# Kernel tuning notes

Measured on AMD Instinct MI355X. Metric: run time of the kernel, lower is better.

## Reference

```python
import jax, jax.numpy as jnp
import numpy as np

S = 16384          # vision tokens (one image, 128x128 patches)
HID = 1280         # vision_hidden_size
H = 16             # num heads
D = HID // H       # head_dim = 80
L = 8              # vision_depth
FF = 3456          # vision_intermediate_size
WIN = 64           # tokens per attention window
UNIT = 4           # spatial_merge_size ** 2
OUT = 2048         # vision_out_hidden_size
PV = 3 * 2 * 16 * 16  # patch volume = 1536


def setup_inputs() -> dict:
    keys = iter(jax.random.split(jax.random.key(0), 32))
    def nrm(shape, fan_in):
        return jax.random.normal(next(keys), shape, jnp.float32) * (fan_in ** -0.5)
    ang = jax.random.uniform(next(keys), (S, D // 2), jnp.float32, 0.0, 2.0 * float(np.pi))
    ang = jnp.concatenate([ang, ang], axis=-1)  # rotate_half-compatible duplicated layout
    return {
        "x": jax.random.normal(next(keys), (S, PV), jnp.float32),
        "cos": jnp.cos(ang), "sin": jnp.sin(ang),
        "cu_seqlens": jnp.arange(S // WIN + 1, dtype=jnp.int32) * WIN,
        "pe_w": nrm((PV, HID), PV), "pe_b": jnp.zeros((HID,), jnp.float32),
        "ln1_w": jnp.ones((L, HID), jnp.float32), "ln1_b": jnp.zeros((L, HID), jnp.float32),
        "qkv_w": nrm((L, HID, 3 * HID), HID), "qkv_b": jnp.zeros((L, 3 * HID), jnp.float32),
        "proj_w": nrm((L, HID, HID), HID), "proj_b": jnp.zeros((L, HID), jnp.float32),
        "ln2_w": jnp.ones((L, HID), jnp.float32), "ln2_b": jnp.zeros((L, HID), jnp.float32),
        "fc1_w": nrm((L, HID, FF), HID), "fc1_b": jnp.zeros((L, FF), jnp.float32),
        "fc2_w": nrm((L, FF, HID), FF), "fc2_b": jnp.zeros((L, HID), jnp.float32),
        "m_ln_w": jnp.ones((HID,), jnp.float32), "m_ln_b": jnp.zeros((HID,), jnp.float32),
        "m_fc1_w": nrm((UNIT * HID, UNIT * HID), UNIT * HID), "m_fc1_b": jnp.zeros((UNIT * HID,), jnp.float32),
        "m_fc2_w": nrm((UNIT * HID, OUT), UNIT * HID), "m_fc2_b": jnp.zeros((OUT,), jnp.float32),
    }


def _ln(t, w, b, eps=1e-6):
    m = jnp.mean(t, axis=-1, keepdims=True)
    v = jnp.mean((t - m) ** 2, axis=-1, keepdims=True)
    return (t - m) * jax.lax.rsqrt(v + eps) * w + b


def _forward(cu_seqlens, x, cos, sin, pe_w, pe_b, ln1_w, ln1_b, qkv_w, qkv_b,
             proj_w, proj_b, ln2_w, ln2_b, fc1_w, fc1_b, fc2_w, fc2_b,
             m_ln_w, m_ln_b, m_fc1_w, m_fc1_b, m_fc2_w, m_fc2_b):
    NW = cu_seqlens.shape[0] - 1  # uniform windows (static)
    W = S // NW
    scale = D ** -0.5
    cosr = cos[:, None, :]  # [S,1,D]
    sinr = sin[:, None, :]

    def rope(t):  # t: [S,H,D]
        t1, t2 = jnp.split(t, 2, axis=-1)
        return t * cosr + jnp.concatenate((-t2, t1), axis=-1) * sinr

    h = x @ pe_w + pe_b  # patch embed: [S, HID]

    def block(h, p):
        l1w, l1b, qw, qb, pw, pb, l2w, l2b, f1w, f1b, f2w, f2b = p
        xn = _ln(h, l1w, l1b)
        q, k, v = jnp.split(xn @ qw + qb, 3, axis=-1)
        q = rope(q.reshape(S, H, D))
        k = rope(k.reshape(S, H, D))
        v = v.reshape(S, H, D)
        # block-diagonal (windowed) attention, fp32 scores as in source
        qw_ = q.reshape(NW, W, H, D)
        kw_ = k.reshape(NW, W, H, D)
        vw_ = v.reshape(NW, W, H, D)
        scores = jnp.einsum('wqhd,wkhd->whqk', qw_, kw_) * scale
        attn = jnp.einsum('whqk,wkhd->wqhd', jax.nn.softmax(scores, axis=-1), vw_)
        h = h + (attn.reshape(S, HID) @ pw + pb)
        xn2 = _ln(h, l2w, l2b)
        h = h + (jax.nn.gelu(xn2 @ f1w + f1b, approximate=True) @ f2w + f2b)
        return h, None

    h, _ = jax.lax.scan(block, h, (ln1_w, ln1_b, qkv_w, qkv_b, proj_w, proj_b,
                                   ln2_w, ln2_b, fc1_w, fc1_b, fc2_w, fc2_b))
    # patch merger (pre-shuffle norm)
    hm = _ln(h, m_ln_w, m_ln_b).reshape(-1, UNIT * HID)  # [S/4, 5120]
    return jax.nn.gelu(hm @ m_fc1_w + m_fc1_b, approximate=True) @ m_fc2_w + m_fc2_b


def reference(x, cos, sin, cu_seqlens, pe_w, pe_b, ln1_w, ln1_b, qkv_w, qkv_b,
              proj_w, proj_b, ln2_w, ln2_b, fc1_w, fc1_b, fc2_w, fc2_b,
              m_ln_w, m_ln_b, m_fc1_w, m_fc1_b, m_fc2_w, m_fc2_b):
    return _forward(cu_seqlens, x, cos, sin, pe_w, pe_b, ln1_w, ln1_b, qkv_w, qkv_b,
                    proj_w, proj_b, ln2_w, ln2_b, fc1_w, fc1_b, fc2_w, fc2_b,
                    m_ln_w, m_ln_b, m_fc1_w, m_fc1_b, m_fc2_w, m_fc2_b)
```

## Files before the change

### kernel.cpp

```cpp
#include <hip/hip_runtime.h>

typedef unsigned short ushortT;
typedef __attribute__((ext_vector_type(8))) short short8;
typedef __attribute__((ext_vector_type(8))) unsigned short ushort8;
typedef __attribute__((ext_vector_type(4))) unsigned short ushort4v;
typedef __attribute__((ext_vector_type(4))) float f32x4;

#define DEVINL __device__ __forceinline__

DEVINL ushortT f2bf(float f) {
    unsigned u = __builtin_bit_cast(unsigned, f);
    u += 0x7FFFu + ((u >> 16) & 1u);
    return (ushortT)(u >> 16);
}
DEVINL float bf2f(ushortT h) {
    unsigned u = ((unsigned)h) << 16;
    return __builtin_bit_cast(float, u);
}
DEVINL float gelu_tanh(float x) {
    float x3 = x * x * x;
    return 0.5f * x * (1.0f + tanhf(0.7978845608028654f * (x + 0.044715f * x3)));
}

#define GLOAD_LDS16(g, l)                                                     \
    __builtin_amdgcn_global_load_lds(                                         \
        (const __attribute__((address_space(1))) void*)(g),                   \
        (__attribute__((address_space(3))) void*)(l), 16, 0, 0)

__global__ __launch_bounds__(256) void cast_bf16_4(const float* __restrict__ in,
                                                   ushortT* __restrict__ out, long n4) {
    long i = (long)blockIdx.x * 256 + threadIdx.x;
    if (i < n4) {
        const float* p = in + i * 4;
        ushort4v o;
        o[0] = f2bf(p[0]); o[1] = f2bf(p[1]); o[2] = f2bf(p[2]); o[3] = f2bf(p[3]);
        ((ushort4v*)out)[i] = o;
    }
}

__global__ __launch_bounds__(256) void transpose_cast(const float* __restrict__ in,
                                                      ushortT* __restrict__ out,
                                                      int K, int N, int Npad) {
    __shared__ float tile[32][33];
    long zi = (long)blockIdx.z * K * N;
    long zo = (long)blockIdx.z * Npad * K;
    const float* ip = in + zi;
    ushortT* op = out + zo;
    int t = threadIdx.x, bx = blockIdx.x, by = blockIdx.y;
#pragma unroll
    for (int i = 0; i < 4; i++) {
        int idx = i * 256 + t, r = idx >> 5, c = idx & 31;
        int col = bx * 32 + c;
        tile[r][c] = (col < N) ? ip[(long)(by * 32 + r) * N + col] : 0.0f;
    }
    __syncthreads();
#pragma unroll
    for (int i = 0; i < 4; i++) {
        int idx = i * 256 + t, r = idx >> 5, c = idx & 31;
        op[(long)(bx * 32 + r) * K + by * 32 + c] = f2bf(tile[c][r]);
    }
}

__global__ __launch_bounds__(256) void pad_bias(const float* __restrict__ in,
                                                float* __restrict__ out,
                                                int n_in, int n_out, int total) {
    int i = blockIdx.x * 256 + threadIdx.x;
    if (i < total) {
        int l = i / n_out, c = i % n_out;
        out[i] = (c < n_in) ? in[l * n_in + c] : 0.0f;
    }
}

__global__ __launch_bounds__(256) void ln_to_bf16(const float* __restrict__ in,
                                                  const float* __restrict__ w,
                                                  const float* __restrict__ b,
                                                  ushortT* __restrict__ out) {
    const int row = blockIdx.x;
    const float* x = in + (long)row * 1280;
    __shared__ float red[4];
    float v[5];
    float s = 0.f;
#pragma unroll
    for (int i = 0; i < 5; i++) { v[i] = x[threadIdx.x + i * 256]; s += v[i]; }
#pragma unroll
    for (int o = 32; o > 0; o >>= 1) s += __shfl_xor(s, o);
    int wave = threadIdx.x >> 6;
    if ((threadIdx.x & 63) == 0) red[wave] = s;
    __syncthreads();
    float mean = (red[0] + red[1] + red[2] + red[3]) * (1.0f / 1280.0f);
    float q = 0.f;
#pragma unroll
    for (int i = 0; i < 5; i++) { float d = v[i] - mean; q += d * d; }
#pragma unroll
    for (int o = 32; o > 0; o >>= 1) q += __shfl_xor(q, o);
    __syncthreads();
    if ((threadIdx.x & 63) == 0) red[wave] = q;
    __syncthreads();
    float var = (red[0] + red[1] + red[2] + red[3]) * (1.0f / 1280.0f);
    float rs = rsqrtf(var + 1e-6f);
#pragma unroll
    for (int i = 0; i < 5; i++) {
        int c = threadIdx.x + i * 256;
        out[(long)row * 1280 + c] = f2bf((v[i] - mean) * rs * w[c] + b[c]);
    }
}

template <int BM, int BN, int WN, bool OBF, bool RES, bool GEL>
__global__ __launch_bounds__(128 * WN, WN == 4 ? 2 : 3)
void gemm2ph(const ushortT* __restrict__ A, const ushortT* __restrict__ Bt,
             const float* __restrict__ bias, const float* __restrict__ res,
             void* __restrict__ out, int M, int N, int K, int lda, int ldb) {
    constexpr int THREADS = 128 * WN;
    constexpr int MR = BM / 32;
    constexpr int NR = BN / (WN * 16);
    constexpr int AOPS = (BM * 8) / THREADS;
    constexpr int BOPS = (BN * 8) / THREADS;
    __shared__ ushortT lsA[2][BM * 64];
    __shared__ ushortT lsB[2][BN * 64];

    const int t = threadIdx.x;
    const int lane = t & 63, lr = lane & 15, lg = lane >> 4;
    const int wave = t >> 6;
    const int wr = wave / WN, wc = wave % WN;

    const int nwg = gridDim.x;
    const int orig = blockIdx.x;
    const int q = nwg >> 3, r8 = nwg & 7;
    const int xcd = orig & 7, loc = orig >> 3;
    const int wg = (xcd < r8 ? xcd * (q + 1) : r8 * (q + 1) + (xcd - r8) * q) + loc;
    const int gx = N / BN;
    const int bx = wg % gx, by = wg / gx;
    const long brow = (long)by * BM;
    const long bcol = (long)bx * BN;

    auto stage = [&](int buf, int k0) {
#pragma unroll
        for (int j = 0; j < AOPS; j++) {
            int idx = j * THREADS + t;
            int row = idx >> 3, slot = idx & 7;
            int ss = slot ^ (row & 7);
            GLOAD_LDS16(A + (size_t)(brow + row) * lda + k0 + ss * 8,
                        &lsA[buf][idx * 8]);
        }
#pragma unroll
        for (int j = 0; j < BOPS; j++) {
            int idx = j * THREADS + t;
            int row = idx >> 3, slot = idx & 7;
            int ss = slot ^ (row & 7);
            GLOAD_LDS16(Bt + (size_t)(bcol + row) * ldb + k0 + ss * 8,
                        &lsB[buf][idx * 8]);
        }
    };

    f32x4 acc[MR][NR];
#pragma unroll
    for (int m = 0; m < MR; m++)
#pragma unroll
        for (int n = 0; n < NR; n++) acc[m][n] = f32x4{0.f, 0.f, 0.f, 0.f};

    stage(0, 0);
    __syncthreads();

    const int NT = K >> 6;
    for (int tt = 0; tt < NT; tt++) {
        const int cur = tt & 1;
        if (tt + 1 < NT) stage(cur ^ 1, (tt + 1) << 6);
#pragma unroll
        for (int kk = 0; kk < 2; kk++) {
            short8 af[MR], bfg[NR];
#pragma unroll
            for (int m = 0; m < MR; m++) {
                int row = wr * (BM / 2) + m * 16 + lr;
                af[m] = *(const short8*)&lsA[cur][row * 64 + (((kk * 4 + lg) ^ (row & 7)) * 8)];
            }
#pragma unroll
            for (int n = 0; n < NR; n++) {
                int row = wc * (BN / WN) + n * 16 + lr;
                bfg[n] = *(const short8*)&lsB[cur][row * 64 + (((kk * 4 + lg) ^ (row & 7)) * 8)];
            }
#pragma unroll
            for (int m = 0; m < MR; m++)
#pragma unroll
                for (int n = 0; n < NR; n++)
                    acc[m][n] = __builtin_amdgcn_mfma_f32_16x16x32_bf16(af[m], bfg[n],
                                                                        acc[m][n], 0, 0, 0);
        }
        __syncthreads();
    }

#pragma unroll
    for (int m = 0; m < MR; m++) {
#pragma unroll
        for (int n = 0; n < NR; n++) {
#pragma unroll
            for (int rr = 0; rr < 4; rr++) {
                size_t row = brow + wr * (BM / 2) + m * 16 + lg * 4 + rr;
                size_t col = bcol + wc * (BN / WN) + n * 16 + lr;
                float v = acc[m][n][rr] + bias[col];
                if (RES) v += res[row * N + col];
                if (GEL) v = gelu_tanh(v);
                if (OBF) ((ushortT*)out)[row * N + col] = f2bf(v);
                else     ((float*)out)[row * N + col] = v;
            }
        }
    }
}

__global__ __launch_bounds__(256) void attn_win(const ushortT* __restrict__ qkv,
                                                const float* __restrict__ cosb,
                                                const float* __restrict__ sinb,
                                                ushortT* __restrict__ out) {
    const int w = blockIdx.x, h = blockIdx.y;
    __shared__ ushortT qs[64 * 96];
    __shared__ ushortT ks[64 * 96];
    __shared__ ushortT vt[80 * 80];
    __shared__ float   sc[64 * 65];
    __shared__ ushortT pb[64 * 80];
    const int t = threadIdx.x, wave = t >> 6, lane = t & 63, lr = lane & 15, lg = lane >> 4;
    const ushortT* bq = qkv + (long)w * 64 * 3840 + h * 80;

    for (int c = t; c < 640; c += 256) {
        int r = c / 10, cb = c % 10;
        const ushortT* qp = bq + (long)r * 3840;
        ushort8 qa = *(const ushort8*)(qp + cb * 8);
        ushort8 ka = *(const ushort8*)(qp + 1280 + cb * 8);
        int pcb = (cb < 5) ? cb + 5 : cb - 5;
        ushort8 qpr = *(const ushort8*)(qp + pcb * 8);
        ushort8 kpr = *(const ushort8*)(qp + 1280 + pcb * 8);
        long srow = (long)w * 64 + r;
        const float* cp = cosb + srow * 80 + cb * 8;
        const float* sp = sinb + srow * 80 + cb * 8;
        float sgn = (cb < 5) ? -1.f : 1.f;
        ushort8 qo, ko;
#pragma unroll
        for (int j = 0; j < 8; j++) {
            float c_ = cp[j], s_ = sp[j] * sgn;
            qo[j] = f2bf(bf2f(qa[j]) * c_ + bf2f(qpr[j]) * s_);
            ko[j] = f2bf(bf2f(ka[j]) * c_ + bf2f(kpr[j]) * s_);
        }
        *(ushort8*)&qs[r * 96 + cb * 8] = qo;
        *(ushort8*)&ks[r * 96 + cb * 8] = ko;
        ushort8 vv = *(const ushort8*)(qp + 2560 + cb * 8);
#pragma unroll
        for (int j = 0; j < 8; j++) vt[(cb * 8 + j) * 80 + r] = vv[j];
    }
    for (int idx = t; idx < 1024; idx += 256) {
        int r = idx >> 4, c2 = 80 + (idx & 15);
        qs[r * 96 + c2] = 0;
        ks[r * 96 + c2] = 0;
    }
    __syncthreads();

    f32x4 sa[4];
#pragma unroll
    for (int n = 0; n < 4; n++) sa[n] = f32x4{0.f, 0.f, 0.f, 0.f};
#pragma unroll
    for (int kk = 0; kk < 3; kk++) {
        short8 aq = *(const short8*)&qs[(wave * 16 + lr) * 96 + kk * 32 + lg * 8];
#pragma unroll
        for (int n = 0; n < 4; n++) {
            short8 bk = *(const short8*)&ks[(n * 16 + lr) * 96 + kk * 32 + lg * 8];
            sa[n] = __builtin_amdgcn_mfma_f32_16x16x32_bf16(aq, bk, sa[n], 0, 0, 0);
        }
    }
    const float scale = 0.11180339887498949f;
#pragma unroll
    for (int n = 0; n < 4; n++)
#pragma unroll
        for (int r = 0; r < 4; r++)
            sc[(wave * 16 + lg * 4 + r) * 65 + n * 16 + lr] = sa[n][r] * scale;
    __syncthreads();

    {
        int row = t >> 2, q4 = t & 3;
        float pv[16];
        float mx = -1e30f;
#pragma unroll
        for (int j = 0; j < 16; j++) { pv[j] = sc[row * 65 + q4 * 16 + j]; mx = fmaxf(mx, pv[j]); }
        mx = fmaxf(mx, __shfl_xor(mx, 1));
        mx = fmaxf(mx, __shfl_xor(mx, 2));
        float sum = 0.f;
#pragma unroll
        for (int j = 0; j < 16; j++) { pv[j] = __expf(pv[j] - mx); sum += pv[j]; }
        sum += __shfl_xor(sum, 1);
        sum += __shfl_xor(sum, 2);
        float inv = 1.0f / sum;
#pragma unroll
        for (int j = 0; j < 16; j++) pb[row * 80 + q4 * 16 + j] = f2bf(pv[j] * inv);
    }
    __syncthreads();

    f32x4 pa[5];
#pragma unroll
    for (int n = 0; n < 5; n++) pa[n] = f32x4{0.f, 0.f, 0.f, 0.f};
#pragma unroll
    for (int kk = 0; kk < 2; kk++) {
        short8 ap = *(const short8*)&pb[(wave * 16 + lr) * 80 + kk * 32 + lg * 8];
#pragma unroll
        for (int n = 0; n < 5; n++) {
            short8 bv = *(const short8*)&vt[(n * 16 + lr) * 80 + kk * 32 + lg * 8];
            pa[n] = __builtin_amdgcn_mfma_f32_16x16x32_bf16(ap, bv, pa[n], 0, 0, 0);
        }
    }
    ushortT* ob = out + (long)w * 64 * 1280 + h * 80;
#pragma unroll
    for (int n = 0; n < 5; n++)
#pragma unroll
        for (int r = 0; r < 4; r++)
            ob[(long)(wave * 16 + lg * 4 + r) * 1280 + n * 16 + lr] = f2bf(pa[n][r]);
}

extern "C" void kernel_launch(void* const* d_in, const int* in_sizes, int n_in,
                              void* d_out, int out_size, void* d_ws, size_t ws_size,
                              hipStream_t stream) {
    const float* x      = (const float*)d_in[0];
    const float* cosb   = (const float*)d_in[1];
    const float* sinb   = (const float*)d_in[2];
    const float* pe_w   = (const float*)d_in[4];
    const float* pe_b   = (const float*)d_in[5];
    const float* ln1_w  = (const float*)d_in[6];
    const float* ln1_b  = (const float*)d_in[7];
    const float* qkv_w  = (const float*)d_in[8];
    const float* qkv_b  = (const float*)d_in[9];
    const float* proj_w = (const float*)d_in[10];
    const float* proj_b = (const float*)d_in[11];
    const float* ln2_w  = (const float*)d_in[12];
    const float* ln2_b  = (const float*)d_in[13];
    const float* fc1_w  = (const float*)d_in[14];
    const float* fc1_b  = (const float*)d_in[15];
    const float* fc2_w  = (const float*)d_in[16];
    const float* fc2_b  = (const float*)d_in[17];
    const float* mln_w  = (const float*)d_in[18];
    const float* mln_b  = (const float*)d_in[19];
    const float* mfc1_w = (const float*)d_in[20];
    const float* mfc1_b = (const float*)d_in[21];
    const float* mfc2_w = (const float*)d_in[22];
    const float* mfc2_b = (const float*)d_in[23];

    char* ws = (char*)d_ws;
    size_t off = 0;
    auto alloc = [&](size_t bytes) -> char* {
        char* p = ws + off;
        off += (bytes + 255) & ~(size_t)255;
        return p;
    };
    ushortT* pe_wT   = (ushortT*)alloc((size_t)1280 * 1536 * 2);
    ushortT* qkv_wT  = (ushortT*)alloc((size_t)8 * 3840 * 1280 * 2);
    ushortT* proj_wT = (ushortT*)alloc((size_t)8 * 1280 * 1280 * 2);
    ushortT* fc1_wT  = (ushortT*)alloc((size_t)8 * 3584 * 1280 * 2);
    ushortT* fc2_wT  = (ushortT*)alloc((size_t)8 * 1280 * 3456 * 2);
    ushortT* mfc1_wT = (ushortT*)alloc((size_t)5120 * 5120 * 2);
    ushortT* mfc2_wT = (ushortT*)alloc((size_t)2048 * 5120 * 2);
    float*   fc1_bp  = (float*)alloc((size_t)8 * 3584 * 4);
    float*   hbuf    = (float*)alloc((size_t)16384 * 1280 * 4);
    ushortT* xn      = (ushortT*)alloc((size_t)16384 * 1280 * 2);
    ushortT* big     = (ushortT*)alloc((size_t)16384 * 3840 * 2);
    ushortT* attnb   = (ushortT*)alloc((size_t)16384 * 1280 * 2);

    ushortT* xbf  = big;
    ushortT* qkvb = big;
    ushortT* ffn1 = big;
    ushortT* t1   = attnb;

    transpose_cast<<<dim3(1280 / 32, 1536 / 32, 1), 256, 0, stream>>>(pe_w,   pe_wT,   1536, 1280, 1280);
    transpose_cast<<<dim3(3840 / 32, 1280 / 32, 8), 256, 0, stream>>>(qkv_w,  qkv_wT,  1280, 3840, 3840);
    transpose_cast<<<dim3(1280 / 32, 1280 / 32, 8), 256, 0, stream>>>(proj_w, proj_wT, 1280, 1280, 1280);
    transpose_cast<<<dim3(3584 / 32, 1280 / 32, 8), 256, 0, stream>>>(fc1_w,  fc1_wT,  1280, 3456, 3584);
    transpose_cast<<<dim3(1280 / 32, 3456 / 32, 8), 256, 0, stream>>>(fc2_w,  fc2_wT,  3456, 1280, 1280);
    transpose_cast<<<dim3(5120 / 32, 5120 / 32, 1), 256, 0, stream>>>(mfc1_w, mfc1_wT, 5120, 5120, 5120);
    transpose_cast<<<dim3(2048 / 32, 5120 / 32, 1), 256, 0, stream>>>(mfc2_w, mfc2_wT, 5120, 2048, 2048);
    pad_bias<<<(8 * 3584 + 255) / 256, 256, 0, stream>>>(fc1_b, fc1_bp, 3456, 3584, 8 * 3584);

    cast_bf16_4<<<(16384L * 1536 / 4 + 255) / 256, 256, 0, stream>>>(x, xbf, 16384L * 1536 / 4);
    gemm2ph<128, 128, 2, false, false, false><<<dim3(10 * 128), 256, 0, stream>>>(
        xbf, pe_wT, pe_b, nullptr, hbuf, 16384, 1280, 1536, 1536, 1536);

    for (int l = 0; l < 8; l++) {
        ln_to_bf16<<<16384, 256, 0, stream>>>(hbuf, ln1_w + l * 1280, ln1_b + l * 1280, xn);
        gemm2ph<256, 256, 4, true, false, false><<<dim3(15 * 64), 512, 0, stream>>>(
            xn, qkv_wT + (size_t)l * 3840 * 1280, qkv_b + l * 3840, nullptr, qkvb,
            16384, 3840, 1280, 1280, 1280);
        attn_win<<<dim3(256, 16), 256, 0, stream>>>(qkvb, cosb, sinb, attnb);
        gemm2ph<128, 128, 2, false, true, false><<<dim3(10 * 128), 256, 0, stream>>>(
            attnb, proj_wT + (size_t)l * 1280 * 1280, proj_b + l * 1280, hbuf, hbuf,
            16384, 1280, 1280, 1280, 1280);
        ln_to_bf16<<<16384, 256, 0, stream>>>(hbuf, ln2_w + l * 1280, ln2_b + l * 1280, xn);
        gemm2ph<256, 256, 4, true, false, true><<<dim3(14 * 64), 512, 0, stream>>>(
            xn, fc1_wT + (size_t)l * 3584 * 1280, fc1_bp + l * 3584, nullptr, ffn1,
            16384, 3584, 1280, 1280, 1280);
        gemm2ph<128, 128, 2, false, true, false><<<dim3(10 * 128), 256, 0, stream>>>(
            ffn1, fc2_wT + (size_t)l * 1280 * 3456, fc2_b + l * 1280, hbuf, hbuf,
            16384, 1280, 3456, 3584, 3456);
    }

    ln_to_bf16<<<16384, 256, 0, stream>>>(hbuf, mln_w, mln_b, xn);
    gemm2ph<128, 128, 2, true, false, true><<<dim3(40 * 32), 256, 0, stream>>>(
        xn, mfc1_wT, mfc1_b, nullptr, t1, 4096, 5120, 5120, 5120, 5120);
    gemm2ph<128, 128, 2, false, false, false><<<dim3(16 * 32), 256, 0, stream>>>(
        t1, mfc2_wT, mfc2_b, nullptr, (float*)d_out, 4096, 2048, 5120, 5120, 5120);
}
```

Before: 7.741 ms.

## Replace GEMM with 8-phase pipelined 256x256 kernel using fine-grained waits

Replaces the double-buffered gemm2ph template with a fixed 256x256 tile, 8-wave kernel. The K-loop is split into four quarter-phases that interleave half-tile global-to-LDS loads with MFMA work, using explicit vmcnt/lgkmcnt waits, raw barriers, sched barriers and setprio around the MFMA bursts. All GEMMs, including the N=1280 and N=2048 ones, now use 256x256 tiles. This hides load latency better but cuts the grid size for the narrow GEMMs (320 or 128 workgroups), which risks poorer CU occupancy on those launches.

```diff
diff --git a/kernel.cpp b/kernel.cpp
--- a/kernel.cpp
+++ b/kernel.cpp
@@ -26,6 +26,12 @@
     __builtin_amdgcn_global_load_lds(                                         \
         (const __attribute__((address_space(1))) void*)(g),                   \
         (__attribute__((address_space(3))) void*)(l), 16, 0, 0)
+
+#define WAITV(n) asm volatile("s_waitcnt vmcnt(" #n ")" ::: "memory")
+#define LGKM0() asm volatile("s_waitcnt lgkmcnt(0)" ::: "memory")
+#define MEMFENCE() asm volatile("" ::: "memory")
+#define BAR() __builtin_amdgcn_s_barrier()
+#define SCHEDBAR() __builtin_amdgcn_sched_barrier(0)
 
 __global__ __launch_bounds__(256) void cast_bf16_4(const float* __restrict__ in,
                                                    ushortT* __restrict__ out, long n4) {
@@ -105,97 +111,128 @@
     }
 }
 
-template <int BM, int BN, int WN, bool OBF, bool RES, bool GEL>
-__global__ __launch_bounds__(128 * WN, WN == 4 ? 2 : 3)
-void gemm2ph(const ushortT* __restrict__ A, const ushortT* __restrict__ Bt,
+
+#define STAGE_A(buf, half, k0)                                                \
+    _Pragma("unroll") for (int j = 0; j < 2; j++) {                           \
+        int c = j * 512 + t; int sr = c >> 3, slot = c & 7;                   \
+        size_t grow = (size_t)((sr & 63) + ((sr >> 6) << 7) + (half) * 64);   \
+        GLOAD_LDS16(A + (brow + grow) * lda + (k0) + ((slot ^ (sr & 7)) * 8), \
+                    &lsA[buf][(half) * 8192 + c * 8]);                        \
+    }
+#define STAGE_B(buf, half, k0)                                                \
+    _Pragma("unroll") for (int j = 0; j < 2; j++) {                           \
+        int c = j * 512 + t; int sr = c >> 3, slot = c & 7;                   \
+        size_t grow = (size_t)((sr & 31) + ((sr >> 5) << 6) + (half) * 32);   \
+        GLOAD_LDS16(Bt + (bcol + grow) * ldb + (k0) + ((slot ^ (sr & 7)) * 8),\
+                    &lsB[buf][(half) * 8192 + c * 8]);                        \
+    }
+#define READ_A(half)                                                          \
+    _Pragma("unroll") for (int m = 0; m < 4; m++)                             \
+    _Pragma("unroll") for (int kk = 0; kk < 2; kk++) {                        \
+        int sr = wr * 64 + m * 16 + lr;                                       \
+        aF[m][kk] = *(const short8*)&lsA[p][(half) * 8192 + sr * 64 +         \
+                                            (((kk * 4 + lg) ^ (sr & 7)) * 8)];\
+    }
+#define READ_B(nbase)                                                         \
+    _Pragma("unroll") for (int n = 0; n < 2; n++)                             \
+    _Pragma("unroll") for (int kk = 0; kk < 2; kk++) {                        \
+        int sr = wc * 32 + n * 16 + lr;                                       \
+        bF[(nbase) + n][kk] = *(const short8*)&lsB[p][((nbase) >> 1) * 8192 + \
+                                sr * 64 + (((kk * 4 + lg) ^ (sr & 7)) * 8)];  \
+    }
+#define MFMA_Q(half, nbase)                                                   \
+    __builtin_amdgcn_s_setprio(1);                                            \
+    _Pragma("unroll") for (int kk = 0; kk < 2; kk++)                          \
+    _Pragma("unroll") for (int m = 0; m < 4; m++)                             \
+    _Pragma("unroll") for (int n = 0; n < 2; n++)                             \
+        acc[(half) * 4 + m][(nbase) + n] = __builtin_amdgcn_mfma_f32_16x16x32_bf16( \
+            aF[m][kk], bF[(nbase) + n][kk], acc[(half) * 4 + m][(nbase) + n], 0, 0, 0); \
+    __builtin_amdgcn_s_setprio(0);
+
+#define PRE_MFMA() BAR(); LGKM0(); SCHEDBAR()
+
+template <bool OBF, bool RES, bool GEL>
+__global__ __launch_bounds__(512, 2)
+void gemm8ph(const ushortT* __restrict__ A, const ushortT* __restrict__ Bt,
              const float* __restrict__ bias, const float* __restrict__ res,
              void* __restrict__ out, int M, int N, int K, int lda, int ldb) {
-    constexpr int THREADS = 128 * WN;
-    constexpr int MR = BM / 32;
-    constexpr int NR = BN / (WN * 16);
-    constexpr int AOPS = (BM * 8) / THREADS;
-    constexpr int BOPS = (BN * 8) / THREADS;
-    __shared__ ushortT lsA[2][BM * 64];
-    __shared__ ushortT lsB[2][BN * 64];
-
+    __shared__ ushortT lsA[2][16384];
+    __shared__ ushortT lsB[2][16384];
     const int t = threadIdx.x;
     const int lane = t & 63, lr = lane & 15, lg = lane >> 4;
     const int wave = t >> 6;
-    const int wr = wave / WN, wc = wave % WN;
-
-    const int nwg = gridDim.x;
-    const int orig = blockIdx.x;
+    const int wr = wave >> 2, wc = wave & 3;
+
+    const int nwg = gridDim.x, orig = blockIdx.x;
     const int q = nwg >> 3, r8 = nwg & 7;
     const int xcd = orig & 7, loc = orig >> 3;
     const int wg = (xcd < r8 ? xcd * (q + 1) : r8 * (q + 1) + (xcd - r8) * q) + loc;
-    const int gx = N / BN;
-    const int bx = wg % gx, by = wg / gx;
-    const long brow = (long)by * BM;
-    const long bcol = (long)bx * BN;
-
-    auto stage = [&](int buf, int k0) {
-#pragma unroll
-        for (int j = 0; j < AOPS; j++) {
-            int idx = j * THREADS + t;
-            int row = idx >> 3, slot = idx & 7;
-            int ss = slot ^ (row & 7);
-            GLOAD_LDS16(A + (size_t)(brow + row) * lda + k0 + ss * 8,
-                        &lsA[buf][idx * 8]);
-        }
-#pragma unroll
-        for (int j = 0; j < BOPS; j++) {
-            int idx = j * THREADS + t;
-            int row = idx >> 3, slot = idx & 7;
-            int ss = slot ^ (row & 7);
-            GLOAD_LDS16(Bt + (size_t)(bcol + row) * ldb + k0 + ss * 8,
-                        &lsB[buf][idx * 8]);
-        }
-    };
-
-    f32x4 acc[MR][NR];
-#pragma unroll
-    for (int m = 0; m < MR; m++)
-#pragma unroll
-        for (int n = 0; n < NR; n++) acc[m][n] = f32x4{0.f, 0.f, 0.f, 0.f};
-
-    stage(0, 0);
-    __syncthreads();
-
+    const int gx = N >> 8;
+    const size_t brow = (size_t)(wg / gx) * 256;
+    const size_t bcol = (size_t)(wg % gx) * 256;
+
+    f32x4 acc[8][4];
+#pragma unroll
+    for (int m = 0; m < 8; m++)
+#pragma unroll
+        for (int n = 0; n < 4; n++) acc[m][n] = f32x4{0.f, 0.f, 0.f, 0.f};
+
+    STAGE_A(0, 0, 0);
+    STAGE_B(0, 0, 0);
+    STAGE_A(0, 1, 0);
+    STAGE_B(0, 1, 0);
+    WAITV(4); BAR(); MEMFENCE();
+
+    short8 aF[4][2], bF[4][2];
     const int NT = K >> 6;
-    for (int tt = 0; tt < NT; tt++) {
-        const int cur = tt & 1;
-        if (tt + 1 < NT) stage(cur ^ 1, (tt + 1) << 6);
-#pragma unroll
-        for (int kk = 0; kk < 2; kk++) {
-            short8 af[MR], bfg[NR];
-#pragma unroll
-            for (int m = 0; m < MR; m++) {
-                int row = wr * (BM / 2) + m * 16 + lr;
-                af[m] = *(const short8*)&lsA[cur][row * 64 + (((kk * 4 + lg) ^ (row & 7)) * 8)];
-            }
-#pragma unroll
-            for (int n = 0; n < NR; n++) {
-                int row = wc * (BN / WN) + n * 16 + lr;
-                bfg[n] = *(const short8*)&lsB[cur][row * 64 + (((kk * 4 + lg) ^ (row & 7)) * 8)];
-            }
-#pragma unroll
-            for (int m = 0; m < MR; m++)
-#pragma unroll
-                for (int n = 0; n < NR; n++)
-                    acc[m][n] = __builtin_amdgcn_mfma_f32_16x16x32_bf16(af[m], bfg[n],
-                                                                        acc[m][n], 0, 0, 0);
-        }
-        __syncthreads();
-    }
-
-#pragma unroll
-    for (int m = 0; m < MR; m++) {
-#pragma unroll
-        for (int n = 0; n < NR; n++) {
+    int p = 0;
+    for (int tt = 0; tt < NT - 1; ++tt) {
+        const int k1 = (tt + 1) << 6;
+        READ_A(0); READ_B(0);
+        STAGE_A(p ^ 1, 0, k1);
+        PRE_MFMA();
+        MFMA_Q(0, 0);
+        WAITV(4); BAR(); MEMFENCE();
+        READ_A(1);
+        STAGE_B(p ^ 1, 0, k1);
+        PRE_MFMA();
+        MFMA_Q(1, 0);
+        WAITV(4); BAR(); MEMFENCE();
+        READ_B(2);
+        STAGE_A(p ^ 1, 1, k1);
+        PRE_MFMA();
+        MFMA_Q(1, 2);
+        BAR(); MEMFENCE();
+        READ_A(0);
+        STAGE_B(p ^ 1, 1, k1);
+        PRE_MFMA();
+        MFMA_Q(0, 2);
+        WAITV(4); BAR(); MEMFENCE();
+        p ^= 1;
+    }
+    READ_A(0); READ_B(0);
+    PRE_MFMA();
+    MFMA_Q(0, 0);
+    WAITV(2); BAR(); MEMFENCE();
+    READ_A(1);
+    PRE_MFMA();
+    MFMA_Q(1, 0);
+    WAITV(0); BAR(); MEMFENCE();
+    READ_B(2);
+    PRE_MFMA();
+    MFMA_Q(1, 2);
+    READ_A(0);
+    LGKM0(); SCHEDBAR();
+    MFMA_Q(0, 2);
+
+#pragma unroll
+    for (int m = 0; m < 8; m++) {
+#pragma unroll
+        for (int n = 0; n < 4; n++) {
 #pragma unroll
             for (int rr = 0; rr < 4; rr++) {
-                size_t row = brow + wr * (BM / 2) + m * 16 + lg * 4 + rr;
-                size_t col = bcol + wc * (BN / WN) + n * 16 + lr;
+                size_t row = brow + wr * 128 + m * 16 + lg * 4 + rr;
+                size_t col = bcol + wc * 64 + n * 16 + lr;
                 float v = acc[m][n][rr] + bias[col];
                 if (RES) v += res[row * N + col];
                 if (GEL) v = gelu_tanh(v);
@@ -372,30 +409,30 @@
     pad_bias<<<(8 * 3584 + 255) / 256, 256, 0, stream>>>(fc1_b, fc1_bp, 3456, 3584, 8 * 3584);
 
     cast_bf16_4<<<(16384L * 1536 / 4 + 255) / 256, 256, 0, stream>>>(x, xbf, 16384L * 1536 / 4);
-    gemm2ph<128, 128, 2, false, false, false><<<dim3(10 * 128), 256, 0, stream>>>(
+    gemm8ph<false, false, false><<<dim3(5 * 64), 512, 0, stream>>>(
         xbf, pe_wT, pe_b, nullptr, hbuf, 16384, 1280, 1536, 1536, 1536);
 
     for (int l = 0; l < 8; l++) {
         ln_to_bf16<<<16384, 256, 0, stream>>>(hbuf, ln1_w + l * 1280, ln1_b + l * 1280, xn);
-        gemm2ph<256, 256, 4, true, false, false><<<dim3(15 * 64), 512, 0, stream>>>(
+        gemm8ph<true, false, false><<<dim3(15 * 64), 512, 0, stream>>>(
             xn, qkv_wT + (size_t)l * 3840 * 1280, qkv_b + l * 3840, nullptr, qkvb,
             16384, 3840, 1280, 1280, 1280);
         attn_win<<<dim3(256, 16), 256, 0, stream>>>(qkvb, cosb, sinb, attnb);
-        gemm2ph<128, 128, 2, false, true, false><<<dim3(10 * 128), 256, 0, stream>>>(
+        gemm8ph<false, true, false><<<dim3(5 * 64), 512, 0, stream>>>(
             attnb, proj_wT + (size_t)l * 1280 * 1280, proj_b + l * 1280, hbuf, hbuf,
             16384, 1280, 1280, 1280, 1280);
         ln_to_bf16<<<16384, 256, 0, stream>>>(hbuf, ln2_w + l * 1280, ln2_b + l * 1280, xn);
-        gemm2ph<256, 256, 4, true, false, true><<<dim3(14 * 64), 512, 0, stream>>>(
+        gemm8ph<true, false, true><<<dim3(14 * 64), 512, 0, stream>>>(
             xn, fc1_wT + (size_t)l * 3584 * 1280, fc1_bp + l * 3584, nullptr, ffn1,
             16384, 3584, 1280, 1280, 1280);
-        gemm2ph<128, 128, 2, false, true, false><<<dim3(10 * 128), 256, 0, stream>>>(
+        gemm8ph<false, true, false><<<dim3(5 * 64), 512, 0, stream>>>(
             ffn1, fc2_wT + (size_t)l * 1280 * 3456, fc2_b + l * 1280, hbuf, hbuf,
             16384, 1280, 3456, 3584, 3456);
     }
 
     ln_to_bf16<<<16384, 256, 0, stream>>>(hbuf, mln_w, mln_b, xn);
-    gemm2ph<128, 128, 2, true, false, true><<<dim3(40 * 32), 256, 0, stream>>>(
+    gemm8ph<true, false, true><<<dim3(20 * 16), 512, 0, stream>>>(
         xn, mfc1_wT, mfc1_b, nullptr, t1, 4096, 5120, 5120, 5120, 5120);
-    gemm2ph<128, 128, 2, false, false, false><<<dim3(16 * 32), 256, 0, stream>>>(
+    gemm8ph<false, false, false><<<dim3(8 * 16), 512, 0, stream>>>(
         t1, mfc2_wT, mfc2_b, nullptr, (float*)d_out, 4096, 2048, 5120, 5120, 5120);
 }
```

Result: slower. 8.042 ms (+3.9%).

## Rewrite GEMMs with four-stage LDS pipeline, explicit waitcnt and split barriers

Applied to the files above, without the earlier changes.

Replaces the templated double-buffered GEMM with two specialized kernels, one with 256x256 tiles and one with 128x128 tiles. Both use a four-buffer ring with K-step 32, keeping three global-to-LDS loads in flight under manual s_waitcnt vmcnt control. The big kernel also interleaves half the fragment reads and B staging between two MFMA phases, with raw s_barrier calls and s_setprio around MFMA bursts. The swizzle changes to suit 32-wide rows. The aim is to hide global load latency and keep the matrix units busy, at the cost of more fragile hand-written synchronization and more barriers per K-step.

```diff
diff --git a/kernel.cpp b/kernel.cpp
--- a/kernel.cpp
+++ b/kernel.cpp
@@ -26,6 +26,11 @@
     __builtin_amdgcn_global_load_lds(                                         \
         (const __attribute__((address_space(1))) void*)(g),                   \
         (__attribute__((address_space(3))) void*)(l), 16, 0, 0)
+
+#define WAITV(n) asm volatile("s_waitcnt vmcnt(" #n ")" ::: "memory")
+#define MEMFENCE() asm volatile("" ::: "memory")
+#define BAR() __builtin_amdgcn_s_barrier()
+#define BARF() MEMFENCE(); BAR(); MEMFENCE()
 
 __global__ __launch_bounds__(256) void cast_bf16_4(const float* __restrict__ in,
                                                    ushortT* __restrict__ out, long n4) {
@@ -105,97 +110,196 @@
     }
 }
 
-template <int BM, int BN, int WN, bool OBF, bool RES, bool GEL>
-__global__ __launch_bounds__(128 * WN, WN == 4 ? 2 : 3)
-void gemm2ph(const ushortT* __restrict__ A, const ushortT* __restrict__ Bt,
-             const float* __restrict__ bias, const float* __restrict__ res,
-             void* __restrict__ out, int M, int N, int K, int lda, int ldb) {
-    constexpr int THREADS = 128 * WN;
-    constexpr int MR = BM / 32;
-    constexpr int NR = BN / (WN * 16);
-    constexpr int AOPS = (BM * 8) / THREADS;
-    constexpr int BOPS = (BN * 8) / THREADS;
-    __shared__ ushortT lsA[2][BM * 64];
-    __shared__ ushortT lsB[2][BN * 64];
-
+
+#define BSTAGE(mat, ls, base, ld, k0, buf)                                    \
+    _Pragma("unroll") for (int j = 0; j < 2; j++) {                           \
+        int c = j * 512 + t; int sr = c >> 2, sl = c & 3;                     \
+        GLOAD_LDS16(mat + (base + sr) * ld + (k0) + ((sl ^ ((sr >> 1) & 3)) * 8), \
+                    &ls[buf][c * 8]);                                         \
+    }
+#define BREAD_A(mbase)                                                        \
+    _Pragma("unroll") for (int m = 0; m < 4; m++) {                           \
+        int r = wr * 128 + ((mbase) + m) * 16 + lr;                           \
+        aF[m] = *(const short8*)&lsA[rbuf][r * 32 + ((lg ^ ((r >> 1) & 3)) * 8)]; \
+    }
+#define BREAD_B()                                                             \
+    _Pragma("unroll") for (int n = 0; n < 4; n++) {                           \
+        int r = wc * 64 + n * 16 + lr;                                        \
+        bF[n] = *(const short8*)&lsB[rbuf][r * 32 + ((lg ^ ((r >> 1) & 3)) * 8)]; \
+    }
+#define BMFMA(mbase)                                                          \
+    __builtin_amdgcn_s_setprio(1);                                            \
+    _Pragma("unroll") for (int m = 0; m < 4; m++)                             \
+    _Pragma("unroll") for (int n = 0; n < 4; n++)                             \
+        acc[(mbase) + m][n] = __builtin_amdgcn_mfma_f32_16x16x32_bf16(        \
+            aF[m], bF[n], acc[(mbase) + m][n], 0, 0, 0);                      \
+    __builtin_amdgcn_s_setprio(0);
+
+#define BITER(WAITCODE, DOSTAGE)                                              \
+    {                                                                         \
+        const int rbuf = tt & 3, sbuf = (tt + 3) & 3;                         \
+        const int k3 = (tt + 3) << 5;                                         \
+        MEMFENCE();                                                           \
+        BREAD_A(0); BREAD_B();                                                \
+        if (DOSTAGE) { BSTAGE(A, lsA, brow, lda, k3, sbuf); }                 \
+        BARF();                                                               \
+        BMFMA(0);                                                             \
+        BARF();                                                               \
+        BREAD_A(4);                                                           \
+        if (DOSTAGE) { BSTAGE(Bt, lsB, bcol, ldb, k3, sbuf); }                \
+        WAITCODE;                                                             \
+        BARF();                                                               \
+        BMFMA(4);                                                             \
+        BARF();                                                               \
+    }
+
+template <bool OBF, bool RES, bool GEL>
+__global__ __launch_bounds__(512, 2)
+void gemm_big(const ushortT* __restrict__ A, const ushortT* __restrict__ Bt,
+              const float* __restrict__ bias, const float* __restrict__ res,
+              void* __restrict__ out, int M, int N, int K, int lda, int ldb) {
+    __shared__ ushortT lsA[4][8192];
+    __shared__ ushortT lsB[4][8192];
     const int t = threadIdx.x;
     const int lane = t & 63, lr = lane & 15, lg = lane >> 4;
     const int wave = t >> 6;
-    const int wr = wave / WN, wc = wave % WN;
-
-    const int nwg = gridDim.x;
-    const int orig = blockIdx.x;
+    const int wr = wave >> 2, wc = wave & 3;
+
+    const int nwg = gridDim.x, orig = blockIdx.x;
     const int q = nwg >> 3, r8 = nwg & 7;
     const int xcd = orig & 7, loc = orig >> 3;
     const int wg = (xcd < r8 ? xcd * (q + 1) : r8 * (q + 1) + (xcd - r8) * q) + loc;
-    const int gx = N / BN;
-    const int bx = wg % gx, by = wg / gx;
-    const long brow = (long)by * BM;
-    const long bcol = (long)bx * BN;
-
-    auto stage = [&](int buf, int k0) {
-#pragma unroll
-        for (int j = 0; j < AOPS; j++) {
-            int idx = j * THREADS + t;
-            int row = idx >> 3, slot = idx & 7;
-            int ss = slot ^ (row & 7);
-            GLOAD_LDS16(A + (size_t)(brow + row) * lda + k0 + ss * 8,
-                        &lsA[buf][idx * 8]);
+    const int gx = N >> 8;
+    const size_t brow = (size_t)(wg / gx) * 256;
+    const size_t bcol = (size_t)(wg % gx) * 256;
+
+    f32x4 acc[8][4];
+#pragma unroll
+    for (int m = 0; m < 8; m++)
+#pragma unroll
+        for (int n = 0; n < 4; n++) acc[m][n] = f32x4{0.f, 0.f, 0.f, 0.f};
+
+#pragma unroll
+    for (int i = 0; i < 3; i++) {
+        BSTAGE(A, lsA, brow, lda, i << 5, i);
+        BSTAGE(Bt, lsB, bcol, ldb, i << 5, i);
+    }
+    WAITV(8); BARF();
+
+    short8 aF[4], bF[4];
+    const int NT = K >> 5;
+    int tt = 0;
+    for (; tt < NT - 3; ++tt) BITER(WAITV(8), true);
+    BITER(WAITV(4), false); ++tt;
+    BITER(WAITV(0), false); ++tt;
+    BITER((void)0, false);
+
+#pragma unroll
+    for (int m = 0; m < 8; m++) {
+#pragma unroll
+        for (int n = 0; n < 4; n++) {
+#pragma unroll
+            for (int rr = 0; rr < 4; rr++) {
+                size_t row = brow + wr * 128 + m * 16 + lg * 4 + rr;
+                size_t col = bcol + wc * 64 + n * 16 + lr;
+                float v = acc[m][n][rr] + bias[col];
+                if (RES) v += res[row * N + col];
+                if (GEL) v = gelu_tanh(v);
+                if (OBF) ((ushortT*)out)[row * N + col] = f2bf(v);
+                else     ((float*)out)[row * N + col] = v;
+            }
         }
-#pragma unroll
-        for (int j = 0; j < BOPS; j++) {
-            int idx = j * THREADS + t;
-            int row = idx >> 3, slot = idx & 7;
-            int ss = slot ^ (row & 7);
-            GLOAD_LDS16(Bt + (size_t)(bcol + row) * ldb + k0 + ss * 8,
-                        &lsB[buf][idx * 8]);
-        }
-    };
-
-    f32x4 acc[MR][NR];
-#pragma unroll
-    for (int m = 0; m < MR; m++)
-#pragma unroll
-        for (int n = 0; n < NR; n++) acc[m][n] = f32x4{0.f, 0.f, 0.f, 0.f};
-
-    stage(0, 0);
-    __syncthreads();
-
-    const int NT = K >> 6;
-    for (int tt = 0; tt < NT; tt++) {
-        const int cur = tt & 1;
-        if (tt + 1 < NT) stage(cur ^ 1, (tt + 1) << 6);
-#pragma unroll
-        for (int kk = 0; kk < 2; kk++) {
-            short8 af[MR], bfg[NR];
-#pragma unroll
-            for (int m = 0; m < MR; m++) {
-                int row = wr * (BM / 2) + m * 16 + lr;
-                af[m] = *(const short8*)&lsA[cur][row * 64 + (((kk * 4 + lg) ^ (row & 7)) * 8)];
-            }
-#pragma unroll
-            for (int n = 0; n < NR; n++) {
-                int row = wc * (BN / WN) + n * 16 + lr;
-                bfg[n] = *(const short8*)&lsB[cur][row * 64 + (((kk * 4 + lg) ^ (row & 7)) * 8)];
-            }
-#pragma unroll
-            for (int m = 0; m < MR; m++)
-#pragma unroll
-                for (int n = 0; n < NR; n++)
-                    acc[m][n] = __builtin_amdgcn_mfma_f32_16x16x32_bf16(af[m], bfg[n],
-                                                                        acc[m][n], 0, 0, 0);
-        }
-        __syncthreads();
-    }
-
-#pragma unroll
-    for (int m = 0; m < MR; m++) {
-#pragma unroll
-        for (int n = 0; n < NR; n++) {
+    }
+}
+
+#define SSTAGE(mat, ls, base, ld, k0, buf)                                    \
+    _Pragma("unroll") for (int j = 0; j < 2; j++) {                           \
+        int c = j * 256 + t; int sr = c >> 2, sl = c & 3;                     \
+        GLOAD_LDS16(mat + (base + sr) * ld + (k0) + ((sl ^ ((sr >> 1) & 3)) * 8), \
+                    &ls[buf][c * 8]);                                         \
+    }
+#define SREAD()                                                               \
+    _Pragma("unroll") for (int m = 0; m < 4; m++) {                           \
+        int r = wr * 64 + m * 16 + lr;                                        \
+        aF[m] = *(const short8*)&lsA[rbuf][r * 32 + ((lg ^ ((r >> 1) & 3)) * 8)]; \
+    }                                                                         \
+    _Pragma("unroll") for (int n = 0; n < 4; n++) {                           \
+        int r = wc * 64 + n * 16 + lr;                                        \
+        bF[n] = *(const short8*)&lsB[rbuf][r * 32 + ((lg ^ ((r >> 1) & 3)) * 8)]; \
+    }
+#define SMFMA()                                                               \
+    __builtin_amdgcn_s_setprio(1);                                            \
+    _Pragma("unroll") for (int m = 0; m < 4; m++)                             \
+    _Pragma("unroll") for (int n = 0; n < 4; n++)                             \
+        acc[m][n] = __builtin_amdgcn_mfma_f32_16x16x32_bf16(                  \
+            aF[m], bF[n], acc[m][n], 0, 0, 0);                                \
+    __builtin_amdgcn_s_setprio(0);
+
+#define SITER(WAITCODE, DOSTAGE)                                              \
+    {                                                                         \
+        const int rbuf = tt & 3, sbuf = (tt + 3) & 3;                         \
+        const int k3 = (tt + 3) << 5;                                         \
+        MEMFENCE();                                                           \
+        SREAD();                                                              \
+        if (DOSTAGE) {                                                        \
+            SSTAGE(A, lsA, brow, lda, k3, sbuf);                              \
+            SSTAGE(Bt, lsB, bcol, ldb, k3, sbuf);                             \
+        }                                                                     \
+        WAITCODE;                                                             \
+        BARF();                                                               \
+        SMFMA();                                                              \
+        BARF();                                                               \
+    }
+
+template <bool OBF, bool RES, bool GEL>
+__global__ __launch_bounds__(256, 2)
+void gemm_small(const ushortT* __restrict__ A, const ushortT* __restrict__ Bt,
+                const float* __restrict__ bias, const float* __restrict__ res,
+                void* __restrict__ out, int M, int N, int K, int lda, int ldb) {
+    __shared__ ushortT lsA[4][4096];
+    __shared__ ushortT lsB[4][4096];
+    const int t = threadIdx.x;
+    const int lane = t & 63, lr = lane & 15, lg = lane >> 4;
+    const int wave = t >> 6;
+    const int wr = wave >> 1, wc = wave & 1;
+
+    const int nwg = gridDim.x, orig = blockIdx.x;
+    const int q = nwg >> 3, r8 = nwg & 7;
+    const int xcd = orig & 7, loc = orig >> 3;
+    const int wg = (xcd < r8 ? xcd * (q + 1) : r8 * (q + 1) + (xcd - r8) * q) + loc;
+    const int gx = N >> 7;
+    const size_t brow = (size_t)(wg / gx) * 128;
+    const size_t bcol = (size_t)(wg % gx) * 128;
+
+    f32x4 acc[4][4];
+#pragma unroll
+    for (int m = 0; m < 4; m++)
+#pragma unroll
+        for (int n = 0; n < 4; n++) acc[m][n] = f32x4{0.f, 0.f, 0.f, 0.f};
+
+#pragma unroll
+    for (int i = 0; i < 3; i++) {
+        SSTAGE(A, lsA, brow, lda, i << 5, i);
+        SSTAGE(Bt, lsB, bcol, ldb, i << 5, i);
+    }
+    WAITV(8); BARF();
+
+    short8 aF[4], bF[4];
+    const int NT = K >> 5;
+    int tt = 0;
+    for (; tt < NT - 3; ++tt) SITER(WAITV(8), true);
+    SITER(WAITV(4), false); ++tt;
+    SITER(WAITV(0), false); ++tt;
+    SITER((void)0, false);
+
+#pragma unroll
+    for (int m = 0; m < 4; m++) {
+#pragma unroll
+        for (int n = 0; n < 4; n++) {
 #pragma unroll
             for (int rr = 0; rr < 4; rr++) {
-                size_t row = brow + wr * (BM / 2) + m * 16 + lg * 4 + rr;
-                size_t col = bcol + wc * (BN / WN) + n * 16 + lr;
+                size_t row = brow + wr * 64 + m * 16 + lg * 4 + rr;
+                size_t col = bcol + wc * 64 + n * 16 + lr;
                 float v = acc[m][n][rr] + bias[col];
                 if (RES) v += res[row * N + col];
                 if (GEL) v = gelu_tanh(v);
@@ -372,30 +476,30 @@
     pad_bias<<<(8 * 3584 + 255) / 256, 256, 0, stream>>>(fc1_b, fc1_bp, 3456, 3584, 8 * 3584);
 
     cast_bf16_4<<<(16384L * 1536 / 4 + 255) / 256, 256, 0, stream>>>(x, xbf, 16384L * 1536 / 4);
-    gemm2ph<128, 128, 2, false, false, false><<<dim3(10 * 128), 256, 0, stream>>>(
+    gemm_small<false, false, false><<<dim3(128 * 10), 256, 0, stream>>>(
         xbf, pe_wT, pe_b, nullptr, hbuf, 16384, 1280, 1536, 1536, 1536);
 
     for (int l = 0; l < 8; l++) {
         ln_to_bf16<<<16384, 256, 0, stream>>>(hbuf, ln1_w + l * 1280, ln1_b + l * 1280, xn);
-        gemm2ph<256, 256, 4, true, false, false><<<dim3(15 * 64), 512, 0, stream>>>(
+        gemm_big<true, false, false><<<dim3(64 * 15), 512, 0, stream>>>(
             xn, qkv_wT + (size_t)l * 3840 * 1280, qkv_b + l * 3840, nullptr, qkvb,
             16384, 3840, 1280, 1280, 1280);
         attn_win<<<dim3(256, 16), 256, 0, stream>>>(qkvb, cosb, sinb, attnb);
-        gemm2ph<128, 128, 2, false, true, false><<<dim3(10 * 128), 256, 0, stream>>>(
+        gemm_small<false, true, false><<<dim3(128 * 10), 256, 0, stream>>>(
             attnb, proj_wT + (size_t)l * 1280 * 1280, proj_b + l * 1280, hbuf, hbuf,
             16384, 1280, 1280, 1280, 1280);
         ln_to_bf16<<<16384, 256, 0, stream>>>(hbuf, ln2_w + l * 1280, ln2_b + l * 1280, xn);
-        gemm2ph<256, 256, 4, true, false, true><<<dim3(14 * 64), 512, 0, stream>>>(
+        gemm_big<true, false, true><<<dim3(64 * 14), 512, 0, stream>>>(
             xn, fc1_wT + (size_t)l * 3584 * 1280, fc1_bp + l * 3584, nullptr, ffn1,
             16384, 3584, 1280, 1280, 1280);
-        gemm2ph<128, 128, 2, false, true, false><<<dim3(10 * 128), 256, 0, stream>>>(
+        gemm_small<false, true, false><<<dim3(128 * 10), 256, 0, stream>>>(
             ffn1, fc2_wT + (size_t)l * 1280 * 3456, fc2_b + l * 1280, hbuf, hbuf,
             16384, 1280, 3456, 3584, 3456);
     }
 
     ln_to_bf16<<<16384, 256, 0, stream>>>(hbuf, mln_w, mln_b, xn);
-    gemm2ph<128, 128, 2, true, false, true><<<dim3(40 * 32), 256, 0, stream>>>(
+    gemm_small<true, false, true><<<dim3(32 * 40), 256, 0, stream>>>(
         xn, mfc1_wT, mfc1_b, nullptr, t1, 4096, 5120, 5120, 5120, 5120);
-    gemm2ph<128, 128, 2, false, false, false><<<dim3(16 * 32), 256, 0, stream>>>(
+    gemm_small<false, false, false><<<dim3(32 * 16), 256, 0, stream>>>(
         t1, mfc2_wT, mfc2_b, nullptr, (float*)d_out, 4096, 2048, 5120, 5120, 5120);
 }
```

After: 7.469 ms. 1.04x faster.

## Replace GEMM with triple-buffered BK=32 pipeline using manual vmcnt waits

Applied to the files above, without the earlier changes.

Replaces the double-buffered BK=64 templated GEMM with a fixed 128x128 tile, 256-thread kernel that uses a three-stage LDS ring with BK=32. Loads are issued two tiles ahead, and each iteration uses one barrier with explicit s_waitcnt vmcnt instead of __syncthreads. MFMA blocks are bracketed with s_setprio. The QKV and FC1 GEMMs move from 256x256 tiles to 128x128 tiles with more workgroups. The aim is better overlap of global loads with MFMA work and higher occupancy. The cost is lower data reuse per tile on the large GEMMs and more barrier iterations.

```diff
diff --git a/kernel.cpp b/kernel.cpp
--- a/kernel.cpp
+++ b/kernel.cpp
@@ -26,6 +26,11 @@
     __builtin_amdgcn_global_load_lds(                                         \
         (const __attribute__((address_space(1))) void*)(g),                   \
         (__attribute__((address_space(3))) void*)(l), 16, 0, 0)
+
+#define WAITV(n) asm volatile("s_waitcnt vmcnt(" #n ")" ::: "memory")
+#define MEMFENCE() asm volatile("" ::: "memory")
+#define BAR() __builtin_amdgcn_s_barrier()
+#define BARF() MEMFENCE(); BAR(); MEMFENCE()
 
 __global__ __launch_bounds__(256) void cast_bf16_4(const float* __restrict__ in,
                                                    ushortT* __restrict__ out, long n4) {
@@ -105,97 +110,100 @@
     }
 }
 
-template <int BM, int BN, int WN, bool OBF, bool RES, bool GEL>
-__global__ __launch_bounds__(128 * WN, WN == 4 ? 2 : 3)
-void gemm2ph(const ushortT* __restrict__ A, const ushortT* __restrict__ Bt,
+
+#define GSTAGE(mat, ls, base, ld, k0, buf)                                    \
+    _Pragma("unroll") for (int j = 0; j < 2; j++) {                           \
+        int c = j * 256 + t; int sr = c >> 2, sl = c & 3;                     \
+        GLOAD_LDS16(mat + (base + sr) * ld + (k0) + ((sl ^ ((sr >> 1) & 3)) * 8), \
+                    &ls[buf][c * 8]);                                         \
+    }
+#define GREAD()                                                               \
+    _Pragma("unroll") for (int m = 0; m < 4; m++) {                           \
+        int r = wr * 64 + m * 16 + lr;                                        \
+        aF[m] = *(const short8*)&lsA[rbuf][r * 32 + ((lg ^ ((r >> 1) & 3)) * 8)]; \
+    }                                                                         \
+    _Pragma("unroll") for (int n = 0; n < 4; n++) {                           \
+        int r = wc * 64 + n * 16 + lr;                                        \
+        bF[n] = *(const short8*)&lsB[rbuf][r * 32 + ((lg ^ ((r >> 1) & 3)) * 8)]; \
+    }
+#define GMFMA()                                                               \
+    __builtin_amdgcn_s_setprio(1);                                            \
+    _Pragma("unroll") for (int m = 0; m < 4; m++)                             \
+    _Pragma("unroll") for (int n = 0; n < 4; n++)                             \
+        acc[m][n] = __builtin_amdgcn_mfma_f32_16x16x32_bf16(                  \
+            aF[m], bF[n], acc[m][n], 0, 0, 0);                                \
+    __builtin_amdgcn_s_setprio(0);
+
+template <bool OBF, bool RES, bool GEL>
+__global__ __launch_bounds__(256, 3)
+void gemm_r3(const ushortT* __restrict__ A, const ushortT* __restrict__ Bt,
              const float* __restrict__ bias, const float* __restrict__ res,
              void* __restrict__ out, int M, int N, int K, int lda, int ldb) {
-    constexpr int THREADS = 128 * WN;
-    constexpr int MR = BM / 32;
-    constexpr int NR = BN / (WN * 16);
-    constexpr int AOPS = (BM * 8) / THREADS;
-    constexpr int BOPS = (BN * 8) / THREADS;
-    __shared__ ushortT lsA[2][BM * 64];
-    __shared__ ushortT lsB[2][BN * 64];
-
+    __shared__ ushortT lsA[3][4096];
+    __shared__ ushortT lsB[3][4096];
     const int t = threadIdx.x;
     const int lane = t & 63, lr = lane & 15, lg = lane >> 4;
     const int wave = t >> 6;
-    const int wr = wave / WN, wc = wave % WN;
-
-    const int nwg = gridDim.x;
-    const int orig = blockIdx.x;
+    const int wr = wave >> 1, wc = wave & 1;
+
+    const int nwg = gridDim.x, orig = blockIdx.x;
     const int q = nwg >> 3, r8 = nwg & 7;
     const int xcd = orig & 7, loc = orig >> 3;
     const int wg = (xcd < r8 ? xcd * (q + 1) : r8 * (q + 1) + (xcd - r8) * q) + loc;
-    const int gx = N / BN;
-    const int bx = wg % gx, by = wg / gx;
-    const long brow = (long)by * BM;
-    const long bcol = (long)bx * BN;
-
-    auto stage = [&](int buf, int k0) {
-#pragma unroll
-        for (int j = 0; j < AOPS; j++) {
-            int idx = j * THREADS + t;
-            int row = idx >> 3, slot = idx & 7;
-            int ss = slot ^ (row & 7);
-            GLOAD_LDS16(A + (size_t)(brow + row) * lda + k0 + ss * 8,
-                        &lsA[buf][idx * 8]);
-        }
-#pragma unroll
-        for (int j = 0; j < BOPS; j++) {
-            int idx = j * THREADS + t;
-            int row = idx >> 3, slot = idx & 7;
-            int ss = slot ^ (row & 7);
-            GLOAD_LDS16(Bt + (size_t)(bcol + row) * ldb + k0 + ss * 8,
-                        &lsB[buf][idx * 8]);
-        }
-    };
-
-    f32x4 acc[MR][NR];
-#pragma unroll
-    for (int m = 0; m < MR; m++)
-#pragma unroll
-        for (int n = 0; n < NR; n++) acc[m][n] = f32x4{0.f, 0.f, 0.f, 0.f};
-
-    stage(0, 0);
-    __syncthreads();
-
-    const int NT = K >> 6;
-    for (int tt = 0; tt < NT; tt++) {
-        const int cur = tt & 1;
-        if (tt + 1 < NT) stage(cur ^ 1, (tt + 1) << 6);
-#pragma unroll
-        for (int kk = 0; kk < 2; kk++) {
-            short8 af[MR], bfg[NR];
-#pragma unroll
-            for (int m = 0; m < MR; m++) {
-                int row = wr * (BM / 2) + m * 16 + lr;
-                af[m] = *(const short8*)&lsA[cur][row * 64 + (((kk * 4 + lg) ^ (row & 7)) * 8)];
-            }
-#pragma unroll
-            for (int n = 0; n < NR; n++) {
-                int row = wc * (BN / WN) + n * 16 + lr;
-                bfg[n] = *(const short8*)&lsB[cur][row * 64 + (((kk * 4 + lg) ^ (row & 7)) * 8)];
-            }
-#pragma unroll
-            for (int m = 0; m < MR; m++)
-#pragma unroll
-                for (int n = 0; n < NR; n++)
-                    acc[m][n] = __builtin_amdgcn_mfma_f32_16x16x32_bf16(af[m], bfg[n],
-                                                                        acc[m][n], 0, 0, 0);
-        }
-        __syncthreads();
-    }
-
-#pragma unroll
-    for (int m = 0; m < MR; m++) {
-#pragma unroll
-        for (int n = 0; n < NR; n++) {
+    const int gx = N >> 7;
+    const size_t brow = (size_t)(wg / gx) * 128;
+    const size_t bcol = (size_t)(wg % gx) * 128;
+
+    f32x4 acc[4][4];
+#pragma unroll
+    for (int m = 0; m < 4; m++)
+#pragma unroll
+        for (int n = 0; n < 4; n++) acc[m][n] = f32x4{0.f, 0.f, 0.f, 0.f};
+
+    GSTAGE(A, lsA, brow, lda, 0, 0);
+    GSTAGE(Bt, lsB, bcol, ldb, 0, 0);
+    GSTAGE(A, lsA, brow, lda, 32, 1);
+    GSTAGE(Bt, lsB, bcol, ldb, 32, 1);
+    WAITV(4); BARF();
+
+    short8 aF[4], bF[4];
+    const int NT = K >> 5;
+    int tt = 0;
+    for (; tt < NT - 2; ++tt) {
+        const int rbuf = tt % 3, sbuf = (tt + 2) % 3;
+        const int k2 = (tt + 2) << 5;
+        MEMFENCE();
+        GREAD();
+        GSTAGE(A, lsA, brow, lda, k2, sbuf);
+        GSTAGE(Bt, lsB, bcol, ldb, k2, sbuf);
+        WAITV(4);
+        BARF();
+        GMFMA();
+    }
+    {
+        const int rbuf = tt % 3;
+        MEMFENCE();
+        GREAD();
+        WAITV(0);
+        BARF();
+        GMFMA();
+        ++tt;
+    }
+    {
+        const int rbuf = tt % 3;
+        MEMFENCE();
+        GREAD();
+        GMFMA();
+    }
+
+#pragma unroll
+    for (int m = 0; m < 4; m++) {
+#pragma unroll
+        for (int n = 0; n < 4; n++) {
 #pragma unroll
             for (int rr = 0; rr < 4; rr++) {
-                size_t row = brow + wr * (BM / 2) + m * 16 + lg * 4 + rr;
-                size_t col = bcol + wc * (BN / WN) + n * 16 + lr;
+                size_t row = brow + wr * 64 + m * 16 + lg * 4 + rr;
+                size_t col = bcol + wc * 64 + n * 16 + lr;
                 float v = acc[m][n][rr] + bias[col];
                 if (RES) v += res[row * N + col];
                 if (GEL) v = gelu_tanh(v);
@@ -372,30 +380,30 @@
     pad_bias<<<(8 * 3584 + 255) / 256, 256, 0, stream>>>(fc1_b, fc1_bp, 3456, 3584, 8 * 3584);
 
     cast_bf16_4<<<(16384L * 1536 / 4 + 255) / 256, 256, 0, stream>>>(x, xbf, 16384L * 1536 / 4);
-    gemm2ph<128, 128, 2, false, false, false><<<dim3(10 * 128), 256, 0, stream>>>(
+    gemm_r3<false, false, false><<<dim3(128 * 10), 256, 0, stream>>>(
         xbf, pe_wT, pe_b, nullptr, hbuf, 16384, 1280, 1536, 1536, 1536);
 
     for (int l = 0; l < 8; l++) {
         ln_to_bf16<<<16384, 256, 0, stream>>>(hbuf, ln1_w + l * 1280, ln1_b + l * 1280, xn);
-        gemm2ph<256, 256, 4, true, false, false><<<dim3(15 * 64), 512, 0, stream>>>(
+        gemm_r3<true, false, false><<<dim3(128 * 30), 256, 0, stream>>>(
             xn, qkv_wT + (size_t)l * 3840 * 1280, qkv_b + l * 3840, nullptr, qkvb,
             16384, 3840, 1280, 1280, 1280);
         attn_win<<<dim3(256, 16), 256, 0, stream>>>(qkvb, cosb, sinb, attnb);
-        gemm2ph<128, 128, 2, false, true, false><<<dim3(10 * 128), 256, 0, stream>>>(
+        gemm_r3<false, true, false><<<dim3(128 * 10), 256, 0, stream>>>(
             attnb, proj_wT + (size_t)l * 1280 * 1280, proj_b + l * 1280, hbuf, hbuf,
             16384, 1280, 1280, 1280, 1280);
         ln_to_bf16<<<16384, 256, 0, stream>>>(hbuf, ln2_w + l * 1280, ln2_b + l * 1280, xn);
-        gemm2ph<256, 256, 4, true, false, true><<<dim3(14 * 64), 512, 0, stream>>>(
+        gemm_r3<true, false, true><<<dim3(128 * 28), 256, 0, stream>>>(
             xn, fc1_wT + (size_t)l * 3584 * 1280, fc1_bp + l * 3584, nullptr, ffn1,
             16384, 3584, 1280, 1280, 1280);
-        gemm2ph<128, 128, 2, false, true, false><<<dim3(10 * 128), 256, 0, stream>>>(
+        gemm_r3<false, true, false><<<dim3(128 * 10), 256, 0, stream>>>(
             ffn1, fc2_wT + (size_t)l * 1280 * 3456, fc2_b + l * 1280, hbuf, hbuf,
             16384, 1280, 3456, 3584, 3456);
     }
 
     ln_to_bf16<<<16384, 256, 0, stream>>>(hbuf, mln_w, mln_b, xn);
-    gemm2ph<128, 128, 2, true, false, true><<<dim3(40 * 32), 256, 0, stream>>>(
+    gemm_r3<true, false, true><<<dim3(32 * 40), 256, 0, stream>>>(
         xn, mfc1_wT, mfc1_b, nullptr, t1, 4096, 5120, 5120, 5120, 5120);
-    gemm2ph<128, 128, 2, false, false, false><<<dim3(16 * 32), 256, 0, stream>>>(
+    gemm_r3<false, false, false><<<dim3(32 * 16), 256, 0, stream>>>(
         t1, mfc2_wT, mfc2_b, nullptr, (float*)d_out, 4096, 2048, 5120, 5120, 5120);
 }
```

Result: faster. 7.364 ms (-4.9%).
